# Performance work log

Hardware: AMD Instinct MI355X
Metric: run time of the kernel (lower is better)

## Reference

```python
import jax, jax.numpy as jnp
import numpy as np

B, T, C, HS = 4, 4096, 64, 64  # batch, seq (== block_size), num_embedding, head_size


def setup_inputs() -> dict:
    key = jax.random.key(0)
    k1, k2, k3, k4 = jax.random.split(key, 4)
    x = jax.random.normal(k1, (B, T, C), dtype=jnp.float32)
    # nn.Linear(num_embedding, head_size, bias=False) weights, stored as [C, HS]
    # so that projection is x @ W (equivalent to torch's x @ weight.T)
    scale = 1.0 / np.sqrt(C)
    Wq = jax.random.normal(k2, (C, HS), dtype=jnp.float32) * scale
    Wk = jax.random.normal(k3, (C, HS), dtype=jnp.float32) * scale
    Wv = jax.random.normal(k4, (C, HS), dtype=jnp.float32) * scale
    return {"x": x, "Wq": Wq, "Wk": Wk, "Wv": Wv}


def reference(x, Wq, Wk, Wv):
    Bx, Tx, Cx = x.shape
    q = jnp.einsum('btc,ch->bth', x, Wq)
    k = jnp.einsum('btc,ch->bth', x, Wk)
    v = jnp.einsum('btc,ch->bth', x, Wv)
    # NOTE: source multiplies by C**0.5 (quirk of the original code), not 1/sqrt.
    wei = jnp.einsum('bth,bsh->bts', q, k) * (Cx ** 0.5)  # [B,T,T]
    causal = jnp.tril(jnp.ones((Tx, Tx), dtype=bool))
    wei = jnp.where(causal, wei, -jnp.inf)
    wei = jax.nn.softmax(wei, axis=-1)
    return jnp.einsum('bts,bsh->bth', wei, v)
```

## Files before the change

kernel.cpp:

```cpp
#include <hip/hip_runtime.h>
#include <hip/hip_bf16.h>

#define B_ 4
#define T_ 4096

typedef __attribute__((ext_vector_type(8))) short short8;
typedef __attribute__((ext_vector_type(4))) float f32x4;
typedef unsigned short ushort_t;
typedef unsigned int uint32;

__device__ __forceinline__ ushort_t bf16_of(float f) {
    __hip_bfloat16 h = __float2bfloat16(f);
    return __builtin_bit_cast(unsigned short, h);
}

__global__ __launch_bounds__(256) void qkv_proj(
    const float* __restrict__ x, const float* __restrict__ Wq,
    const float* __restrict__ Wk, const float* __restrict__ Wv,
    ushort_t* __restrict__ Qhi, ushort_t* __restrict__ Qlo,
    ushort_t* __restrict__ Khi, ushort_t* __restrict__ Klo,
    ushort_t* __restrict__ Vt)
{
    __shared__ float Ws[3][64][65];
    const int tid = threadIdx.x;
    {
        const float* Wp[3] = {Wq, Wk, Wv};
        for (int mm = 0; mm < 3; ++mm)
            for (int ii = tid; ii < 4096; ii += 256)
                Ws[mm][ii >> 6][ii & 63] = Wp[mm][ii];
    }
    __syncthreads();

    const int w = tid >> 6, lane = tid & 63;
    const int l16 = lane & 15, g = lane >> 4;
    const int R0 = blockIdx.x * 32 + 16 * (w & 1);
    const int h = w >> 1;

    short8 ah[2], al[2];
#pragma unroll
    for (int cc = 0; cc < 2; ++cc) {
        const float* xp = x + (size_t)(R0 + l16) * 64 + cc * 32 + 8 * g;
        float4 v0 = *(const float4*)xp;
        float4 v1 = *(const float4*)(xp + 4);
        float xv[8] = {v0.x, v0.y, v0.z, v0.w, v1.x, v1.y, v1.z, v1.w};
#pragma unroll
        for (int jj = 0; jj < 8; ++jj) {
            __hip_bfloat16 hh = __float2bfloat16(xv[jj]);
            ah[cc][jj] = (short)__builtin_bit_cast(unsigned short, hh);
            al[cc][jj] = (short)bf16_of(xv[jj] - __bfloat162float(hh));
        }
    }

    const float QS = 11.541560327111707f;
#pragma unroll
    for (int u6 = 0; u6 < 6; ++u6) {
        const int u = h * 6 + u6;
        const int mm = u >> 2, ct = u & 3;
        f32x4 d = (f32x4){0.f, 0.f, 0.f, 0.f};
#pragma unroll
        for (int cc = 0; cc < 2; ++cc) {
            short8 bh, bl;
#pragma unroll
            for (int jj = 0; jj < 8; ++jj) {
                float wv = Ws[mm][cc * 32 + 8 * g + jj][ct * 16 + l16];
                __hip_bfloat16 hh = __float2bfloat16(wv);
                bh[jj] = (short)__builtin_bit_cast(unsigned short, hh);
                bl[jj] = (short)bf16_of(wv - __bfloat162float(hh));
            }
            d = __builtin_amdgcn_mfma_f32_16x16x32_bf16(ah[cc], bh, d, 0, 0, 0);
            d = __builtin_amdgcn_mfma_f32_16x16x32_bf16(ah[cc], bl, d, 0, 0, 0);
            d = __builtin_amdgcn_mfma_f32_16x16x32_bf16(al[cc], bh, d, 0, 0, 0);
        }
        const int col = ct * 16 + l16;
        if (mm == 0) {
#pragma unroll
            for (int r = 0; r < 4; ++r) {
                const int R = R0 + 4 * g + r;
                float v = d[r] * QS;
                __hip_bfloat16 hh = __float2bfloat16(v);
                Qhi[(size_t)R * 64 + col] = __builtin_bit_cast(unsigned short, hh);
                Qlo[(size_t)R * 64 + col] = bf16_of(v - __bfloat162float(hh));
            }
        } else if (mm == 1) {
#pragma unroll
            for (int r = 0; r < 4; ++r) {
                const int R = R0 + 4 * g + r;
                float v = d[r];
                __hip_bfloat16 hh = __float2bfloat16(v);
                Khi[(size_t)R * 64 + col] = __builtin_bit_cast(unsigned short, hh);
                Klo[(size_t)R * 64 + col] = bf16_of(v - __bfloat162float(hh));
            }
        } else {
            const int bb = R0 >> 12;
            const int t0 = (R0 & (T_ - 1)) + 4 * g;
            uint32 lo = (uint32)bf16_of(d[0]) | ((uint32)bf16_of(d[1]) << 16);
            uint32 hi = (uint32)bf16_of(d[2]) | ((uint32)bf16_of(d[3]) << 16);
            uint2 pk; pk.x = lo; pk.y = hi;
            *(uint2*)(Vt + ((size_t)(bb * 64 + col)) * T_ + t0) = pk;
        }
    }
}

__global__ __launch_bounds__(256, 2) void flash_attn(
    const ushort_t* __restrict__ Qhi, const ushort_t* __restrict__ Qlo,
    const ushort_t* __restrict__ Khi, const ushort_t* __restrict__ Klo,
    const ushort_t* __restrict__ Vt, float* __restrict__ out)
{
    __shared__ __align__(16) ushort_t Pb[4][2][16][72];
    __shared__ float mrg[2][64][3][26];

    const int tid = threadIdx.x;
    const int p = tid >> 6;
    const int lane = tid & 63;
    const int l16 = lane & 15, g = lane >> 4;

    const int bid = blockIdx.x;
    const int xg = bid & 7;
    const int b = xg & 3;
    const int jj = bid >> 3;
    const int i = (xg >> 2) ? (126 - 2 * jj) : (127 - 2 * jj);
    const int q0 = i * 32;
    const int nkt = (q0 + 32 + 63) >> 6;

    short8 aQh[2][2], aQl[2][2];
#pragma unroll
    for (int su = 0; su < 2; ++su) {
        const size_t qb = ((size_t)(b * T_ + q0 + su * 16 + l16)) * 64;
#pragma unroll
        for (int cc = 0; cc < 2; ++cc) {
            aQh[su][cc] = *(const short8*)(Qhi + qb + cc * 32 + 8 * g);
            aQl[su][cc] = *(const short8*)(Qlo + qb + cc * 32 + 8 * g);
        }
    }

    float m[2][4], lsum[2][4];
    f32x4 acc[2][4];
#pragma unroll
    for (int su = 0; su < 2; ++su)
#pragma unroll
        for (int r = 0; r < 4; ++r) { m[su][r] = -__builtin_inff(); lsum[su][r] = 0.f; }
#pragma unroll
    for (int su = 0; su < 2; ++su)
#pragma unroll
        for (int hs = 0; hs < 4; ++hs) acc[su][hs] = (f32x4){0.f, 0.f, 0.f, 0.f};

    for (int kt = p; kt < nkt; kt += 4) {
        const size_t kb = ((size_t)(b * T_ + kt * 64)) * 64;
        f32x4 sc[2][4];
        __builtin_amdgcn_s_setprio(1);
#pragma unroll
        for (int ks = 0; ks < 4; ++ks) {
            f32x4 a0 = (f32x4){0.f, 0.f, 0.f, 0.f};
            f32x4 a1 = (f32x4){0.f, 0.f, 0.f, 0.f};
#pragma unroll
            for (int cc = 0; cc < 2; ++cc) {
                const size_t ko = kb + ((size_t)(ks * 16 + l16)) * 64 + cc * 32 + 8 * g;
                short8 bh = *(const short8*)(Khi + ko);
                short8 bl = *(const short8*)(Klo + ko);
                a0 = __builtin_amdgcn_mfma_f32_16x16x32_bf16(aQh[0][cc], bh, a0, 0, 0, 0);
                a0 = __builtin_amdgcn_mfma_f32_16x16x32_bf16(aQh[0][cc], bl, a0, 0, 0, 0);
                a0 = __builtin_amdgcn_mfma_f32_16x16x32_bf16(aQl[0][cc], bh, a0, 0, 0, 0);
                a1 = __builtin_amdgcn_mfma_f32_16x16x32_bf16(aQh[1][cc], bh, a1, 0, 0, 0);
                a1 = __builtin_amdgcn_mfma_f32_16x16x32_bf16(aQh[1][cc], bl, a1, 0, 0, 0);
                a1 = __builtin_amdgcn_mfma_f32_16x16x32_bf16(aQl[1][cc], bh, a1, 0, 0, 0);
            }
            sc[0][ks] = a0; sc[1][ks] = a1;
        }
        __builtin_amdgcn_s_setprio(0);
        if (kt == nkt - 1) {
#pragma unroll
            for (int su = 0; su < 2; ++su)
#pragma unroll
                for (int ks = 0; ks < 4; ++ks)
#pragma unroll
                    for (int r = 0; r < 4; ++r) {
                        int key = kt * 64 + ks * 16 + l16;
                        int row = q0 + su * 16 + 4 * g + r;
                        if (key > row) sc[su][ks][r] = -__builtin_inff();
                    }
        }
        float alv[2][4];
#pragma unroll
        for (int su = 0; su < 2; ++su) {
#pragma unroll
            for (int r = 0; r < 4; ++r) {
                float mt = fmaxf(fmaxf(sc[su][0][r], sc[su][1][r]),
                                 fmaxf(sc[su][2][r], sc[su][3][r]));
#pragma unroll
                for (int msk = 1; msk < 16; msk <<= 1) mt = fmaxf(mt, __shfl_xor(mt, msk));
                float mn = fmaxf(m[su][r], mt);
                alv[su][r] = exp2f(m[su][r] - mn);
                m[su][r] = mn;
            }
            float rs[4] = {0.f, 0.f, 0.f, 0.f};
#pragma unroll
            for (int ks = 0; ks < 4; ++ks)
#pragma unroll
                for (int r = 0; r < 4; ++r) {
                    float pv = exp2f(sc[su][ks][r] - m[su][r]);
                    rs[r] += pv;
                    Pb[p][su][4 * g + r][ks * 16 + l16] = bf16_of(pv);
                }
#pragma unroll
            for (int r = 0; r < 4; ++r) {
#pragma unroll
                for (int msk = 1; msk < 16; msk <<= 1) rs[r] += __shfl_xor(rs[r], msk);
                lsum[su][r] = lsum[su][r] * alv[su][r] + rs[r];
            }
#pragma unroll
            for (int hs = 0; hs < 4; ++hs)
#pragma unroll
                for (int r = 0; r < 4; ++r) acc[su][hs][r] *= alv[su][r];
        }
        __builtin_amdgcn_s_setprio(1);
#pragma unroll
        for (int cc = 0; cc < 2; ++cc) {
            short8 ap0 = *(const short8*)&Pb[p][0][l16][cc * 32 + 8 * g];
            short8 ap1 = *(const short8*)&Pb[p][1][l16][cc * 32 + 8 * g];
#pragma unroll
            for (int hs = 0; hs < 4; ++hs) {
                short8 bv = *(const short8*)(Vt + ((size_t)(b * 64 + hs * 16 + l16)) * T_
                                             + kt * 64 + cc * 32 + 8 * g);
                acc[0][hs] = __builtin_amdgcn_mfma_f32_16x16x32_bf16(ap0, bv, acc[0][hs], 0, 0, 0);
                acc[1][hs] = __builtin_amdgcn_mfma_f32_16x16x32_bf16(ap1, bv, acc[1][hs], 0, 0, 0);
            }
        }
        __builtin_amdgcn_s_setprio(0);
    }

    if (p > 0) {
#pragma unroll
        for (int su = 0; su < 2; ++su) {
            float* mp = &mrg[su][lane][p - 1][0];
#pragma unroll
            for (int r = 0; r < 4; ++r) { mp[r] = m[su][r]; mp[4 + r] = lsum[su][r]; }
#pragma unroll
            for (int hs = 0; hs < 4; ++hs)
#pragma unroll
                for (int r = 0; r < 4; ++r) mp[8 + hs * 4 + r] = acc[su][hs][r];
        }
    }
    __syncthreads();
    if (p == 0) {
#pragma unroll
        for (int su = 0; su < 2; ++su) {
#pragma unroll
            for (int r = 0; r < 4; ++r) {
                float mm = m[su][r], ll = lsum[su][r];
                float ac[4];
#pragma unroll
                for (int hs = 0; hs < 4; ++hs) ac[hs] = acc[su][hs][r];
#pragma unroll
                for (int pp = 0; pp < 3; ++pp) {
                    const float* mp = &mrg[su][lane][pp][0];
                    float m1 = mp[r], l1 = mp[4 + r];
                    float mf = fmaxf(mm, m1);
                    float a0 = exp2f(mm - mf);
                    float a1 = exp2f(m1 - mf);
                    ll = ll * a0 + l1 * a1;
#pragma unroll
                    for (int hs = 0; hs < 4; ++hs)
                        ac[hs] = ac[hs] * a0 + mp[8 + hs * 4 + r] * a1;
                    mm = mf;
                }
                float inv = 1.f / ll;
                const size_t ob = ((size_t)(b * T_ + q0 + su * 16 + 4 * g + r)) * 64;
#pragma unroll
                for (int hs = 0; hs < 4; ++hs) out[ob + hs * 16 + l16] = ac[hs] * inv;
            }
        }
    }
}

extern "C" void kernel_launch(void* const* d_in, const int* in_sizes, int n_in,
                              void* d_out, int out_size, void* d_ws, size_t ws_size,
                              hipStream_t stream) {
    const float* x  = (const float*)d_in[0];
    const float* Wq = (const float*)d_in[1];
    const float* Wk = (const float*)d_in[2];
    const float* Wv = (const float*)d_in[3];
    float* out = (float*)d_out;

    const size_t N = (size_t)B_ * T_ * 64;
    ushort_t* Qhi = (ushort_t*)d_ws;
    ushort_t* Qlo = Qhi + N;
    ushort_t* Khi = Qlo + N;
    ushort_t* Klo = Khi + N;
    ushort_t* Vt  = Klo + N;

    qkv_proj<<<512, 256, 0, stream>>>(x, Wq, Wk, Wv, Qhi, Qlo, Khi, Klo, Vt);
    flash_attn<<<512, 256, 0, stream>>>(Qhi, Qlo, Khi, Klo, Vt, out);
}
```

Measured before the change: 158.0 us.

## Stream-K split of causal attention with fp16 MFMA, DPP reductions, and merge pass

```diff
diff --git a/kernel.cpp b/kernel.cpp
--- a/kernel.cpp
+++ b/kernel.cpp
@@ -3,23 +3,45 @@
 
 #define B_ 4
 #define T_ 4096
-
+#define UPB 4160
+#define NB 256
+#define SLOTS 5
+
+typedef _Float16 half_t;
+typedef __attribute__((ext_vector_type(8))) _Float16 half8;
 typedef __attribute__((ext_vector_type(8))) short short8;
 typedef __attribute__((ext_vector_type(4))) float f32x4;
 typedef unsigned short ushort_t;
 typedef unsigned int uint32;
 
-__device__ __forceinline__ ushort_t bf16_of(float f) {
-    __hip_bfloat16 h = __float2bfloat16(f);
+__device__ __forceinline__ ushort_t h_bits(float f) {
+    half_t h = (half_t)f;
     return __builtin_bit_cast(unsigned short, h);
+}
+__device__ __forceinline__ float f_of_h(ushort_t u) {
+    half_t h = __builtin_bit_cast(half_t, u);
+    return (float)h;
+}
+template <int CTRL>
+__device__ __forceinline__ float dpp_fmax(float x) {
+    int xi = __builtin_bit_cast(int, x);
+    int yi = __builtin_amdgcn_update_dpp(xi, xi, CTRL, 0xF, 0xF, false);
+    return fmaxf(x, __builtin_bit_cast(float, yi));
+}
+__device__ __forceinline__ float red16_fmax(float x) {
+    x = dpp_fmax<0xB1>(x);
+    x = dpp_fmax<0x4E>(x);
+    x = dpp_fmax<0x141>(x);
+    x = dpp_fmax<0x140>(x);
+    return x;
 }
 
 __global__ __launch_bounds__(256) void qkv_proj(
     const float* __restrict__ x, const float* __restrict__ Wq,
     const float* __restrict__ Wk, const float* __restrict__ Wv,
-    ushort_t* __restrict__ Qhi, ushort_t* __restrict__ Qlo,
-    ushort_t* __restrict__ Khi, ushort_t* __restrict__ Klo,
-    ushort_t* __restrict__ Vt)
+    half_t* __restrict__ Qh, half_t* __restrict__ Ql,
+    half_t* __restrict__ Kh, half_t* __restrict__ Kl,
+    half_t* __restrict__ Vt)
 {
     __shared__ float Ws[3][64][65];
     const int tid = threadIdx.x;
@@ -36,7 +58,7 @@
     const int R0 = blockIdx.x * 32 + 16 * (w & 1);
     const int h = w >> 1;
 
-    short8 ah[2], al[2];
+    half8 ah[2], al[2];
 #pragma unroll
     for (int cc = 0; cc < 2; ++cc) {
         const float* xp = x + (size_t)(R0 + l16) * 64 + cc * 32 + 8 * g;
@@ -45,9 +67,9 @@
         float xv[8] = {v0.x, v0.y, v0.z, v0.w, v1.x, v1.y, v1.z, v1.w};
 #pragma unroll
         for (int jj = 0; jj < 8; ++jj) {
-            __hip_bfloat16 hh = __float2bfloat16(xv[jj]);
-            ah[cc][jj] = (short)__builtin_bit_cast(unsigned short, hh);
-            al[cc][jj] = (short)bf16_of(xv[jj] - __bfloat162float(hh));
+            half_t hh = (half_t)xv[jj];
+            ah[cc][jj] = hh;
+            al[cc][jj] = (half_t)(xv[jj] - (float)hh);
         }
     }
 
@@ -59,217 +81,290 @@
         f32x4 d = (f32x4){0.f, 0.f, 0.f, 0.f};
 #pragma unroll
         for (int cc = 0; cc < 2; ++cc) {
-            short8 bh, bl;
+            half8 bh, bl;
 #pragma unroll
             for (int jj = 0; jj < 8; ++jj) {
                 float wv = Ws[mm][cc * 32 + 8 * g + jj][ct * 16 + l16];
-                __hip_bfloat16 hh = __float2bfloat16(wv);
-                bh[jj] = (short)__builtin_bit_cast(unsigned short, hh);
-                bl[jj] = (short)bf16_of(wv - __bfloat162float(hh));
-            }
-            d = __builtin_amdgcn_mfma_f32_16x16x32_bf16(ah[cc], bh, d, 0, 0, 0);
-            d = __builtin_amdgcn_mfma_f32_16x16x32_bf16(ah[cc], bl, d, 0, 0, 0);
-            d = __builtin_amdgcn_mfma_f32_16x16x32_bf16(al[cc], bh, d, 0, 0, 0);
+                half_t hh = (half_t)wv;
+                bh[jj] = hh;
+                bl[jj] = (half_t)(wv - (float)hh);
+            }
+            d = __builtin_amdgcn_mfma_f32_16x16x32_f16(ah[cc], bh, d, 0, 0, 0);
+            d = __builtin_amdgcn_mfma_f32_16x16x32_f16(ah[cc], bl, d, 0, 0, 0);
+            d = __builtin_amdgcn_mfma_f32_16x16x32_f16(al[cc], bh, d, 0, 0, 0);
         }
         const int col = ct * 16 + l16;
         if (mm == 0) {
 #pragma unroll
             for (int r = 0; r < 4; ++r) {
-                const int R = R0 + 4 * g + r;
                 float v = d[r] * QS;
-                __hip_bfloat16 hh = __float2bfloat16(v);
-                Qhi[(size_t)R * 64 + col] = __builtin_bit_cast(unsigned short, hh);
-                Qlo[(size_t)R * 64 + col] = bf16_of(v - __bfloat162float(hh));
+                half_t hh = (half_t)v;
+                Qh[(size_t)(R0 + 4 * g + r) * 64 + col] = hh;
+                Ql[(size_t)(R0 + 4 * g + r) * 64 + col] = (half_t)(v - (float)hh);
             }
         } else if (mm == 1) {
 #pragma unroll
             for (int r = 0; r < 4; ++r) {
-                const int R = R0 + 4 * g + r;
                 float v = d[r];
-                __hip_bfloat16 hh = __float2bfloat16(v);
-                Khi[(size_t)R * 64 + col] = __builtin_bit_cast(unsigned short, hh);
-                Klo[(size_t)R * 64 + col] = bf16_of(v - __bfloat162float(hh));
+                half_t hh = (half_t)v;
+                Kh[(size_t)(R0 + 4 * g + r) * 64 + col] = hh;
+                Kl[(size_t)(R0 + 4 * g + r) * 64 + col] = (half_t)(v - (float)hh);
             }
         } else {
             const int bb = R0 >> 12;
             const int t0 = (R0 & (T_ - 1)) + 4 * g;
-            uint32 lo = (uint32)bf16_of(d[0]) | ((uint32)bf16_of(d[1]) << 16);
-            uint32 hi = (uint32)bf16_of(d[2]) | ((uint32)bf16_of(d[3]) << 16);
-            uint2 pk; pk.x = lo; pk.y = hi;
+            uint2 pk;
+            pk.x = (uint32)h_bits(d[0]) | ((uint32)h_bits(d[1]) << 16);
+            pk.y = (uint32)h_bits(d[2]) | ((uint32)h_bits(d[3]) << 16);
             *(uint2*)(Vt + ((size_t)(bb * 64 + col)) * T_ + t0) = pk;
         }
     }
 }
 
-__global__ __launch_bounds__(256, 2) void flash_attn(
-    const ushort_t* __restrict__ Qhi, const ushort_t* __restrict__ Qlo,
-    const ushort_t* __restrict__ Khi, const ushort_t* __restrict__ Klo,
-    const ushort_t* __restrict__ Vt, float* __restrict__ out)
+__global__ __launch_bounds__(256, 4) void flash_sk(
+    const half_t* __restrict__ Qh, const half_t* __restrict__ Ql,
+    const half_t* __restrict__ Kh, const half_t* __restrict__ Kl,
+    const half_t* __restrict__ Vt,
+    ushort_t* __restrict__ PACC, float* __restrict__ PML,
+    float* __restrict__ out)
 {
-    __shared__ __align__(16) ushort_t Pb[4][2][16][72];
-    __shared__ float mrg[2][64][3][26];
+    __shared__ __align__(16) ushort_t Pb[4][16][72];
+    __shared__ float mrgF[2][64][24];
 
     const int tid = threadIdx.x;
-    const int p = tid >> 6;
+    const int wv = tid >> 6;
     const int lane = tid & 63;
     const int l16 = lane & 15, g = lane >> 4;
+    const int su = wv & 1, par = wv >> 1;
 
     const int bid = blockIdx.x;
-    const int xg = bid & 7;
-    const int b = xg & 3;
-    const int jj = bid >> 3;
-    const int i = (xg >> 2) ? (126 - 2 * jj) : (127 - 2 * jj);
-    const int q0 = i * 32;
-    const int nkt = (q0 + 32 + 63) >> 6;
-
-    short8 aQh[2][2], aQl[2][2];
-#pragma unroll
-    for (int su = 0; su < 2; ++su) {
-        const size_t qb = ((size_t)(b * T_ + q0 + su * 16 + l16)) * 64;
-#pragma unroll
-        for (int cc = 0; cc < 2; ++cc) {
-            aQh[su][cc] = *(const short8*)(Qhi + qb + cc * 32 + 8 * g);
-            aQl[su][cc] = *(const short8*)(Qlo + qb + cc * 32 + 8 * g);
-        }
-    }
-
-    float m[2][4], lsum[2][4];
-    f32x4 acc[2][4];
-#pragma unroll
-    for (int su = 0; su < 2; ++su)
-#pragma unroll
-        for (int r = 0; r < 4; ++r) { m[su][r] = -__builtin_inff(); lsum[su][r] = 0.f; }
-#pragma unroll
-    for (int su = 0; su < 2; ++su)
-#pragma unroll
-        for (int hs = 0; hs < 4; ++hs) acc[su][hs] = (f32x4){0.f, 0.f, 0.f, 0.f};
-
-    for (int kt = p; kt < nkt; kt += 4) {
-        const size_t kb = ((size_t)(b * T_ + kt * 64)) * 64;
-        f32x4 sc[2][4];
-        __builtin_amdgcn_s_setprio(1);
-#pragma unroll
-        for (int ks = 0; ks < 4; ++ks) {
-            f32x4 a0 = (f32x4){0.f, 0.f, 0.f, 0.f};
-            f32x4 a1 = (f32x4){0.f, 0.f, 0.f, 0.f};
+    const int xcd = bid & 7;
+    const int b = xcd >> 1;
+    const int rb = ((bid >> 3) << 1) + (xcd & 1);
+
+    half8 ones;
+#pragma unroll
+    for (int jj = 0; jj < 8; ++jj) ones[jj] = (half_t)1.0f;
+
+    int u = (65 * rb) >> 2;
+    const int uEnd = (65 * (rb + 1)) >> 2;
+
+    while (u < uEnd) {
+        const int r = u;
+        int t = (int)sqrtf((float)r);
+        while ((t + 1) * (t + 1) <= r) ++t;
+        while (t * t > r) --t;
+        int i, kt0;
+        if (r < t * t + t) { i = 2 * t - 1; kt0 = r - t * t; }
+        else               { i = 2 * t;     kt0 = r - t * t - t; }
+        const int nkt = (i >> 1) + 1;
+        const int q0 = i * 32;
+        const int rem = nkt - kt0;
+        const int avail = uEnd - u;
+        const int cnt = (rem < avail) ? rem : avail;
+
+        half8 aQh[2], aQl[2];
+        {
+            const size_t qb = ((size_t)(b * T_ + q0 + su * 16 + l16)) * 64;
 #pragma unroll
             for (int cc = 0; cc < 2; ++cc) {
-                const size_t ko = kb + ((size_t)(ks * 16 + l16)) * 64 + cc * 32 + 8 * g;
-                short8 bh = *(const short8*)(Khi + ko);
-                short8 bl = *(const short8*)(Klo + ko);
-                a0 = __builtin_amdgcn_mfma_f32_16x16x32_bf16(aQh[0][cc], bh, a0, 0, 0, 0);
-                a0 = __builtin_amdgcn_mfma_f32_16x16x32_bf16(aQh[0][cc], bl, a0, 0, 0, 0);
-                a0 = __builtin_amdgcn_mfma_f32_16x16x32_bf16(aQl[0][cc], bh, a0, 0, 0, 0);
-                a1 = __builtin_amdgcn_mfma_f32_16x16x32_bf16(aQh[1][cc], bh, a1, 0, 0, 0);
-                a1 = __builtin_amdgcn_mfma_f32_16x16x32_bf16(aQh[1][cc], bl, a1, 0, 0, 0);
-                a1 = __builtin_amdgcn_mfma_f32_16x16x32_bf16(aQl[1][cc], bh, a1, 0, 0, 0);
-            }
-            sc[0][ks] = a0; sc[1][ks] = a1;
-        }
-        __builtin_amdgcn_s_setprio(0);
-        if (kt == nkt - 1) {
-#pragma unroll
-            for (int su = 0; su < 2; ++su)
+                aQh[cc] = *(const half8*)(Qh + qb + cc * 32 + 8 * g);
+                aQl[cc] = *(const half8*)(Ql + qb + cc * 32 + 8 * g);
+            }
+        }
+
+        float m[4], lsum[4];
+        f32x4 acc[4];
+#pragma unroll
+        for (int rr = 0; rr < 4; ++rr) { m[rr] = -__builtin_inff(); lsum[rr] = 0.f; }
+#pragma unroll
+        for (int hs = 0; hs < 4; ++hs) acc[hs] = (f32x4){0.f, 0.f, 0.f, 0.f};
+
+        for (int e = par; e < cnt; e += 2) {
+            const int kt = kt0 + e;
+            const size_t kb = ((size_t)(b * T_ + kt * 64)) * 64;
+            f32x4 sc[4];
+            __builtin_amdgcn_s_setprio(1);
+#pragma unroll
+            for (int ks = 0; ks < 4; ++ks) {
+                f32x4 a = (f32x4){0.f, 0.f, 0.f, 0.f};
+#pragma unroll
+                for (int cc = 0; cc < 2; ++cc) {
+                    const size_t ko = kb + ((size_t)(ks * 16 + l16)) * 64 + cc * 32 + 8 * g;
+                    half8 bh = *(const half8*)(Kh + ko);
+                    half8 bl = *(const half8*)(Kl + ko);
+                    a = __builtin_amdgcn_mfma_f32_16x16x32_f16(aQh[cc], bh, a, 0, 0, 0);
+                    a = __builtin_amdgcn_mfma_f32_16x16x32_f16(aQh[cc], bl, a, 0, 0, 0);
+                    a = __builtin_amdgcn_mfma_f32_16x16x32_f16(aQl[cc], bh, a, 0, 0, 0);
+                }
+                sc[ks] = a;
+            }
+            __builtin_amdgcn_s_setprio(0);
+            if (kt == nkt - 1) {
 #pragma unroll
                 for (int ks = 0; ks < 4; ++ks)
 #pragma unroll
-                    for (int r = 0; r < 4; ++r) {
+                    for (int rr = 0; rr < 4; ++rr) {
                         int key = kt * 64 + ks * 16 + l16;
-                        int row = q0 + su * 16 + 4 * g + r;
-                        if (key > row) sc[su][ks][r] = -__builtin_inff();
+                        int row = q0 + su * 16 + 4 * g + rr;
+                        if (key > row) sc[ks][rr] = -__builtin_inff();
                     }
-        }
-        float alv[2][4];
-#pragma unroll
-        for (int su = 0; su < 2; ++su) {
-#pragma unroll
-            for (int r = 0; r < 4; ++r) {
-                float mt = fmaxf(fmaxf(sc[su][0][r], sc[su][1][r]),
-                                 fmaxf(sc[su][2][r], sc[su][3][r]));
-#pragma unroll
-                for (int msk = 1; msk < 16; msk <<= 1) mt = fmaxf(mt, __shfl_xor(mt, msk));
-                float mn = fmaxf(m[su][r], mt);
-                alv[su][r] = exp2f(m[su][r] - mn);
-                m[su][r] = mn;
-            }
-            float rs[4] = {0.f, 0.f, 0.f, 0.f};
+            }
+            float mt[4];
+#pragma unroll
+            for (int rr = 0; rr < 4; ++rr) {
+                float tmx = fmaxf(fmaxf(sc[0][rr], sc[1][rr]),
+                                  fmaxf(sc[2][rr], sc[3][rr]));
+                mt[rr] = red16_fmax(tmx);
+            }
+            float alv[4];
+            bool grow = (mt[0] > m[0]) | (mt[1] > m[1]) |
+                        (mt[2] > m[2]) | (mt[3] > m[3]);
+            if (__ballot(grow)) {
+#pragma unroll
+                for (int rr = 0; rr < 4; ++rr) {
+                    float mn = fmaxf(m[rr], mt[rr]);
+                    alv[rr] = exp2f(m[rr] - mn);
+                    m[rr] = mn;
+                }
+#pragma unroll
+                for (int hs = 0; hs < 4; ++hs)
+#pragma unroll
+                    for (int rr = 0; rr < 4; ++rr) acc[hs][rr] *= alv[rr];
+            } else {
+#pragma unroll
+                for (int rr = 0; rr < 4; ++rr) alv[rr] = 1.f;
+            }
 #pragma unroll
             for (int ks = 0; ks < 4; ++ks)
 #pragma unroll
-                for (int r = 0; r < 4; ++r) {
-                    float pv = exp2f(sc[su][ks][r] - m[su][r]);
-                    rs[r] += pv;
-                    Pb[p][su][4 * g + r][ks * 16 + l16] = bf16_of(pv);
-                }
-#pragma unroll
-            for (int r = 0; r < 4; ++r) {
-#pragma unroll
-                for (int msk = 1; msk < 16; msk <<= 1) rs[r] += __shfl_xor(rs[r], msk);
-                lsum[su][r] = lsum[su][r] * alv[su][r] + rs[r];
-            }
+                for (int rr = 0; rr < 4; ++rr) {
+                    float pv = exp2f(sc[ks][rr] - m[rr]);
+                    Pb[wv][4 * g + rr][ks * 16 + l16] = h_bits(pv);
+                }
+            f32x4 rs = (f32x4){0.f, 0.f, 0.f, 0.f};
+            __builtin_amdgcn_s_setprio(1);
+#pragma unroll
+            for (int cc = 0; cc < 2; ++cc) {
+                half8 ap = *(const half8*)&Pb[wv][l16][cc * 32 + 8 * g];
+                rs = __builtin_amdgcn_mfma_f32_16x16x32_f16(ap, ones, rs, 0, 0, 0);
+#pragma unroll
+                for (int hs = 0; hs < 4; ++hs) {
+                    half8 bv = *(const half8*)(Vt + ((size_t)(b * 64 + hs * 16 + l16)) * T_
+                                               + kt * 64 + cc * 32 + 8 * g);
+                    acc[hs] = __builtin_amdgcn_mfma_f32_16x16x32_f16(ap, bv, acc[hs], 0, 0, 0);
+                }
+            }
+            __builtin_amdgcn_s_setprio(0);
+#pragma unroll
+            for (int rr = 0; rr < 4; ++rr)
+                lsum[rr] = lsum[rr] * alv[rr] + rs[rr];
+        }
+
+        if (par == 1) {
+            float* mp = &mrgF[su][lane][0];
+#pragma unroll
+            for (int rr = 0; rr < 4; ++rr) { mp[rr] = m[rr]; mp[4 + rr] = lsum[rr]; }
 #pragma unroll
             for (int hs = 0; hs < 4; ++hs)
 #pragma unroll
-                for (int r = 0; r < 4; ++r) acc[su][hs][r] *= alv[su][r];
-        }
-        __builtin_amdgcn_s_setprio(1);
-#pragma unroll
-        for (int cc = 0; cc < 2; ++cc) {
-            short8 ap0 = *(const short8*)&Pb[p][0][l16][cc * 32 + 8 * g];
-            short8 ap1 = *(const short8*)&Pb[p][1][l16][cc * 32 + 8 * g];
-#pragma unroll
-            for (int hs = 0; hs < 4; ++hs) {
-                short8 bv = *(const short8*)(Vt + ((size_t)(b * 64 + hs * 16 + l16)) * T_
-                                             + kt * 64 + cc * 32 + 8 * g);
-                acc[0][hs] = __builtin_amdgcn_mfma_f32_16x16x32_bf16(ap0, bv, acc[0][hs], 0, 0, 0);
-                acc[1][hs] = __builtin_amdgcn_mfma_f32_16x16x32_bf16(ap1, bv, acc[1][hs], 0, 0, 0);
-            }
-        }
-        __builtin_amdgcn_s_setprio(0);
-    }
-
-    if (p > 0) {
-#pragma unroll
-        for (int su = 0; su < 2; ++su) {
-            float* mp = &mrg[su][lane][p - 1][0];
-#pragma unroll
-            for (int r = 0; r < 4; ++r) { mp[r] = m[su][r]; mp[4 + r] = lsum[su][r]; }
-#pragma unroll
-            for (int hs = 0; hs < 4; ++hs)
-#pragma unroll
-                for (int r = 0; r < 4; ++r) mp[8 + hs * 4 + r] = acc[su][hs][r];
-        }
-    }
-    __syncthreads();
-    if (p == 0) {
-#pragma unroll
-        for (int su = 0; su < 2; ++su) {
-#pragma unroll
-            for (int r = 0; r < 4; ++r) {
-                float mm = m[su][r], ll = lsum[su][r];
-                float ac[4];
-#pragma unroll
-                for (int hs = 0; hs < 4; ++hs) ac[hs] = acc[su][hs][r];
-#pragma unroll
-                for (int pp = 0; pp < 3; ++pp) {
-                    const float* mp = &mrg[su][lane][pp][0];
-                    float m1 = mp[r], l1 = mp[4 + r];
-                    float mf = fmaxf(mm, m1);
-                    float a0 = exp2f(mm - mf);
-                    float a1 = exp2f(m1 - mf);
-                    ll = ll * a0 + l1 * a1;
+                for (int rr = 0; rr < 4; ++rr) mp[8 + hs * 4 + rr] = acc[hs][rr];
+        }
+        __syncthreads();
+        if (par == 0) {
+            const float* mp = &mrgF[su][lane][0];
+#pragma unroll
+            for (int rr = 0; rr < 4; ++rr) {
+                float m1 = mp[rr], l1 = mp[4 + rr];
+                float mf = fmaxf(m[rr], m1);
+                float a0 = exp2f(m[rr] - mf);
+                float a1 = exp2f(m1 - mf);
+                lsum[rr] = lsum[rr] * a0 + l1 * a1;
+#pragma unroll
+                for (int hs = 0; hs < 4; ++hs)
+                    acc[hs][rr] = acc[hs][rr] * a0 + mp[8 + hs * 4 + rr] * a1;
+                m[rr] = mf;
+            }
+            const bool full = (kt0 == 0) && (cnt == nkt);
+            if (full) {
+#pragma unroll
+                for (int rr = 0; rr < 4; ++rr) {
+                    float inv = 1.f / lsum[rr];
+                    const size_t ob = ((size_t)(b * T_ + q0 + su * 16 + 4 * g + rr)) * 64;
 #pragma unroll
                     for (int hs = 0; hs < 4; ++hs)
-                        ac[hs] = ac[hs] * a0 + mp[8 + hs * 4 + r] * a1;
-                    mm = mf;
-                }
-                float inv = 1.f / ll;
-                const size_t ob = ((size_t)(b * T_ + q0 + su * 16 + 4 * g + r)) * 64;
-#pragma unroll
-                for (int hs = 0; hs < 4; ++hs) out[ob + hs * 16 + l16] = ac[hs] * inv;
-            }
-        }
-    }
+                        out[ob + hs * 16 + l16] = acc[hs][rr] * inv;
+                }
+            } else {
+                const int mh = i >> 1;
+                const int Si = (i & 1) ? (mh + 1) * (mh + 1) : mh * (mh + 1);
+                const int rbf = (4 * Si + 3) / 65;
+                const int slot = rb - rbf;
+                const int Tid = b * 128 + i;
+                ushort_t* pa = PACC + ((size_t)(Tid * SLOTS + slot)) * 2048;
+                float* pm = PML + ((size_t)(Tid * SLOTS + slot)) * 64;
+#pragma unroll
+                for (int hs = 0; hs < 4; ++hs)
+#pragma unroll
+                    for (int rr = 0; rr < 4; ++rr)
+                        pa[(su * 16 + 4 * g + rr) * 64 + hs * 16 + l16] = h_bits(acc[hs][rr]);
+                if (l16 == 0) {
+#pragma unroll
+                    for (int rr = 0; rr < 4; ++rr) {
+                        const int row = su * 16 + 4 * g + rr;
+                        pm[row * 2] = m[rr];
+                        pm[row * 2 + 1] = lsum[rr];
+                    }
+                }
+            }
+        }
+        __syncthreads();
+        u += cnt;
+    }
+}
+
+__global__ __launch_bounds__(256) void merge_k(
+    const ushort_t* __restrict__ PACC, const float* __restrict__ PML,
+    float* __restrict__ out)
+{
+    const int tid = threadIdx.x;
+    const int Tid = blockIdx.x;
+    const int b = Tid >> 7, i = Tid & 127;
+    const int nkt = (i >> 1) + 1;
+    const int mh = i >> 1;
+    const int Si = (i & 1) ? (mh + 1) * (mh + 1) : mh * (mh + 1);
+    const int rbf = (4 * Si + 3) / 65;
+    const int rbl = (4 * (Si + nkt - 1) + 3) / 65;
+    const int n = rbl - rbf + 1;
+    if (n == 1) return;
+
+    const int row = tid >> 3;
+    const int c0 = (tid & 7) * 8;
+
+    float mm = -__builtin_inff(), ll = 0.f;
+    float ac[8];
+#pragma unroll
+    for (int k2 = 0; k2 < 8; ++k2) ac[k2] = 0.f;
+
+    for (int p = 0; p < n; ++p) {
+        const float* pm = PML + ((size_t)(Tid * SLOTS + p)) * 64 + row * 2;
+        float m1 = pm[0], l1 = pm[1];
+        short8 pv = *(const short8*)(PACC + ((size_t)(Tid * SLOTS + p)) * 2048 + row * 64 + c0);
+        float mf = fmaxf(mm, m1);
+        float a0 = exp2f(mm - mf), a1 = exp2f(m1 - mf);
+        ll = ll * a0 + l1 * a1;
+#pragma unroll
+        for (int k2 = 0; k2 < 8; ++k2)
+            ac[k2] = ac[k2] * a0 + f_of_h((ushort_t)pv[k2]) * a1;
+        mm = mf;
+    }
+    float inv = 1.f / ll;
+    float* op = out + ((size_t)(b * T_ + i * 32 + row)) * 64 + c0;
+    float4 o0, o1;
+    o0.x = ac[0] * inv; o0.y = ac[1] * inv; o0.z = ac[2] * inv; o0.w = ac[3] * inv;
+    o1.x = ac[4] * inv; o1.y = ac[5] * inv; o1.z = ac[6] * inv; o1.w = ac[7] * inv;
+    *(float4*)op = o0;
+    *(float4*)(op + 4) = o1;
 }
 
 extern "C" void kernel_launch(void* const* d_in, const int* in_sizes, int n_in,
@@ -282,12 +377,15 @@
     float* out = (float*)d_out;
 
     const size_t N = (size_t)B_ * T_ * 64;
-    ushort_t* Qhi = (ushort_t*)d_ws;
-    ushort_t* Qlo = Qhi + N;
-    ushort_t* Khi = Qlo + N;
-    ushort_t* Klo = Khi + N;
-    ushort_t* Vt  = Klo + N;
-
-    qkv_proj<<<512, 256, 0, stream>>>(x, Wq, Wk, Wv, Qhi, Qlo, Khi, Klo, Vt);
-    flash_attn<<<512, 256, 0, stream>>>(Qhi, Qlo, Khi, Klo, Vt, out);
-}
+    half_t* Qh = (half_t*)d_ws;
+    half_t* Ql = Qh + N;
+    half_t* Kh = Ql + N;
+    half_t* Kl = Kh + N;
+    half_t* Vt = Kl + N;
+    ushort_t* PACC = (ushort_t*)(Vt + N);
+    float* PML = (float*)(PACC + (size_t)512 * SLOTS * 2048);
+
+    qkv_proj<<<512, 256, 0, stream>>>(x, Wq, Wk, Wv, Qh, Ql, Kh, Kl, Vt);
+    flash_sk<<<4 * NB, 256, 0, stream>>>(Qh, Ql, Kh, Kl, Vt, PACC, PML, out);
+    merge_k<<<512, 256, 0, stream>>>(PACC, PML, out);
+}
```

After: 177.7 us. 12.4% more time.
